# Optimization experiments

Hardware: AMD Instinct MI355X
Metric: run time of the kernel (lower is better)

Reference implementation:

```python
import jax, jax.numpy as jnp
import numpy as np

N = 100000      # nodes
E = 800000      # directed edges
D_IN = 128      # input features (n_inputs)
HIDDEN = 128    # conf['model']['hidden_size']
D_OUT = 2       # conv2 output classes


def setup_inputs() -> dict:
    key = jax.random.key(0)
    k0, k1, k2, k3 = jax.random.split(key, 4)
    x = jax.random.normal(k0, (N, D_IN), dtype=jnp.float32)
    edge_index = jax.random.randint(k1, (2, E), 0, N, dtype=jnp.int32)
    # Glorot-style init for GCNConv weights, zero bias (PyG defaults)
    s1 = float(np.sqrt(6.0 / (D_IN + HIDDEN)))
    s2 = float(np.sqrt(6.0 / (HIDDEN + D_OUT)))
    W1 = jax.random.uniform(k2, (D_IN, HIDDEN), jnp.float32, -s1, s1)
    b1 = jnp.zeros((HIDDEN,), jnp.float32)
    W2 = jax.random.uniform(k3, (HIDDEN, D_OUT), jnp.float32, -s2, s2)
    b2 = jnp.zeros((D_OUT,), jnp.float32)
    return {"x": x, "edge_index": edge_index, "W1": W1, "b1": b1, "W2": W2, "b2": b2}


def gcn_conv(x, src, dst, W, b):
    """PyG GCNConv: add self-loops, symmetric deg^-1/2 A deg^-1/2 normalization."""
    n = x.shape[0]
    h = x @ W                                                   # [N, F_out]
    ones_e = jnp.ones((src.shape[0],), h.dtype)
    # degree with self-loops (init to 1)
    deg = jnp.ones((n,), h.dtype).at[dst].add(ones_e)           # [N]
    dinv = 1.0 / jnp.sqrt(deg)
    norm = (dinv[src] * dinv[dst])[:, None]                     # [E, 1]
    # self-loop contribution: norm_ii = dinv_i^2; then scatter edge messages
    out = (h * (dinv * dinv)[:, None]).at[dst].add(h[src] * norm)
    return out + b


def reference(x, edge_index, W1, b1, W2, b2):
    src, dst = edge_index[0], edge_index[1]
    h = jax.nn.relu(gcn_conv(x, src, dst, W1, b1))
    return gcn_conv(h, src, dst, W2, b2)                        # [N, 2]
```

## Files before the change

kernel.cpp:

```cpp
#include <hip/hip_runtime.h>
#include <hip/hip_bf16.h>


#define D1 128
#define BSH 9
#define BSZ (1 << BSH)
#define CHA 2048

typedef __attribute__((ext_vector_type(8))) short short8;
typedef __attribute__((ext_vector_type(4))) float floatx4;

__device__ __forceinline__ unsigned short f2bf(float f) {
    unsigned u = __float_as_uint(f);
    u += 0x7fff + ((u >> 16) & 1);
    return (unsigned short)(u >> 16);
}
__device__ __forceinline__ float bflo(unsigned u) { return __uint_as_float(u << 16); }
__device__ __forceinline__ float bfhi(unsigned u) { return __uint_as_float(u & 0xffff0000u); }
__device__ __forceinline__ int clampN(int s, int N) {
    return (int)min((unsigned)s, (unsigned)N);
}

__global__ void k_init(const float* __restrict__ W1, unsigned short* __restrict__ W1t,
                       int* __restrict__ bcur, unsigned short* __restrict__ h1s,
                       float* __restrict__ h2s, int N) {
    int i = blockIdx.x * 256 + threadIdx.x;
    if (i < 256) bcur[i] = 0;
    if (i < D1) h1s[(size_t)N * D1 + i] = 0;
    if (i < 2)  h2s[(size_t)N * 2 + i] = 0.f;
    if (i < D1 * D1) {
        int c = i >> 7, k = i & 127;
        W1t[c * D1 + k] = f2bf(W1[k * D1 + c]);
    }
}

__global__ __launch_bounds__(256) void k_binA(
    const int* __restrict__ src, const int* __restrict__ dst,
    int* __restrict__ bcur, unsigned* __restrict__ packed, int E, int nbuck, int CAP)
{
    __shared__ int hist[256];
    __shared__ int cur[256];
    const int t = threadIdx.x;
    const int e0 = blockIdx.x * CHA;
    const int e1 = min(e0 + CHA, E);

    for (int i = t; i < nbuck; i += 256) hist[i] = 0;
    __syncthreads();
    for (int i = e0 + t; i < e1; i += 256)
        atomicAdd(&hist[dst[i] >> BSH], 1);
    __syncthreads();
    for (int i = t; i < nbuck; i += 256)
        cur[i] = (hist[i] > 0) ? atomicAdd(&bcur[i], hist[i]) : 0;
    __syncthreads();
    for (int i = e0 + t; i < e1; i += 256) {
        int d = dst[i];
        int b = d >> BSH;
        int pos = atomicAdd(&cur[b], 1);
        if (pos < CAP)
            packed[(size_t)b * CAP + pos] = ((unsigned)src[i] << BSH) | (unsigned)(d & (BSZ - 1));
    }
}

__global__ __launch_bounds__(512) void k_binB(
    const int* __restrict__ bcur, const unsigned* __restrict__ packed,
    int2* __restrict__ rp, float* __restrict__ dinv,
    int* __restrict__ esrc, int* __restrict__ order, int N, int CAP)
{
    __shared__ int lh[BSZ];
    __shared__ int lcur[BSZ];
    __shared__ int wsum[8];
    __shared__ int dbin[64];
    __shared__ int dcur[64];

    const int t = threadIdx.x;
    const int s = blockIdx.x << BSH;
    const int n = min(BSZ, N - s);
    const int base = blockIdx.x * CAP;
    const int cnt = min(bcur[blockIdx.x], CAP);

    lh[t] = 0;
    if (t < 64) dbin[t] = 0;
    __syncthreads();
    for (int i = t; i < cnt; i += 512)
        atomicAdd(&lh[packed[base + i] & (BSZ - 1)], 1);
    __syncthreads();

    const int deg = lh[t];
    const int pdeg = (deg + 3) & ~3;

    int inc = pdeg;
#pragma unroll
    for (int off = 1; off < 64; off <<= 1) {
        int u = __shfl_up(inc, off);
        if ((t & 63) >= off) inc += u;
    }
    if ((t & 63) == 63) wsum[t >> 6] = inc;
    __syncthreads();
    if (t < 8) {
        int w = wsum[t];
#pragma unroll
        for (int off = 1; off < 8; off <<= 1) {
            int u = __shfl_up(w, off, 8);
            if ((t & 7) >= off) w += u;
        }
        wsum[t] = w;
    }
    __syncthreads();
    int excl = ((t >> 6) ? wsum[(t >> 6) - 1] : 0) + inc - pdeg;

    if (t < n) {
        rp[s + t] = make_int2(base + excl, deg);
        dinv[s + t] = rsqrtf(1.0f + (float)deg);
        atomicAdd(&dbin[63 - min(deg, 63)], 1);
        for (int k = deg; k < pdeg; ++k) {
            int p = excl + k;
            if (p < CAP) esrc[base + p] = N;
        }
    }
    lcur[t] = excl;
    __syncthreads();

    for (int i = t; i < cnt; i += 512) {
        unsigned p = packed[base + i];
        int ld = (int)(p & (BSZ - 1));
        int pos = atomicAdd(&lcur[ld], 1);
        if (pos < CAP) esrc[base + pos] = (int)(p >> BSH);
    }

    __syncthreads();
    if (t < 64) {
        int dv = dbin[t];
        int dinc = dv;
#pragma unroll
        for (int off = 1; off < 64; off <<= 1) {
            int u = __shfl_up(dinc, off);
            if (t >= off) dinc += u;
        }
        dcur[t] = dinc - dv;
    }
    __syncthreads();
    if (t < n) {
        int b = 63 - min(deg, 63);
        int pos = atomicAdd(&dcur[b], 1);
        order[s + pos] = s + t;
    }
}

#define BMM 64
__global__ __launch_bounds__(256) void k_gemm1(
    const float* __restrict__ x, const unsigned short* __restrict__ W1t,
    const float* __restrict__ dinv, unsigned short* __restrict__ h1s, int N)
{
    __shared__ unsigned short Xs[BMM][136];
    __shared__ unsigned short Ws[D1][136];

    const int t = threadIdx.x;
    const int row0 = blockIdx.x * BMM;

#pragma unroll
    for (int i = 0; i < 8; ++i) {
        int idx = t + 256 * i;
        int r = idx >> 4, c8 = idx & 15;
        short8 v = ((const short8*)W1t)[r * 16 + c8];
        *(short8*)&Ws[r][c8 * 8] = v;
    }
#pragma unroll
    for (int i = 0; i < 4; ++i) {
        int idx = t + 256 * i;
        int r = idx >> 4, c8 = idx & 15;
        int row = row0 + r;
        short8 v8 = (short8)0;
        if (row < N) {
            const float* p = x + (size_t)row * D1 + c8 * 8;
            float4 f0 = *(const float4*)p;
            float4 f1 = *(const float4*)(p + 4);
            v8[0] = (short)f2bf(f0.x); v8[1] = (short)f2bf(f0.y);
            v8[2] = (short)f2bf(f0.z); v8[3] = (short)f2bf(f0.w);
            v8[4] = (short)f2bf(f1.x); v8[5] = (short)f2bf(f1.y);
            v8[6] = (short)f2bf(f1.z); v8[7] = (short)f2bf(f1.w);
        }
        *(short8*)&Xs[r][c8 * 8] = v8;
    }
    __syncthreads();

    const int w = t >> 6;
    const int l = t & 63;
    const int m = l & 15;
    const int q = l >> 4;

    floatx4 acc[8];
#pragma unroll
    for (int c = 0; c < 8; ++c) acc[c] = (floatx4)0.0f;

#pragma unroll
    for (int ks = 0; ks < 4; ++ks) {
        short8 a = *(const short8*)&Xs[16 * w + m][ks * 32 + q * 8];
#pragma unroll
        for (int c = 0; c < 8; ++c) {
            short8 b = *(const short8*)&Ws[c * 16 + m][ks * 32 + q * 8];
            acc[c] = __builtin_amdgcn_mfma_f32_16x16x32_bf16(a, b, acc[c], 0, 0, 0);
        }
    }

    __syncthreads();

#pragma unroll
    for (int r = 0; r < 4; ++r) {
        int rt = 16 * w + q * 4 + r;
        int row = row0 + rt;
        float di = (row < N) ? dinv[row] : 0.f;
#pragma unroll
        for (int c = 0; c < 8; ++c)
            Xs[rt][c * 16 + m] = f2bf(acc[c][r] * di);
    }
    __syncthreads();

#pragma unroll
    for (int i = 0; i < 4; ++i) {
        int idx = t + 256 * i;
        int r = idx >> 4, c8 = idx & 15;
        int row = row0 + r;
        if (row < N)
            *(short8*)&h1s[(size_t)row * D1 + c8 * 8] = *(const short8*)&Xs[r][c8 * 8];
    }
}

#define ACC8(A, v) \
    A[0] += bflo(v.x); A[1] += bfhi(v.x); \
    A[2] += bflo(v.y); A[3] += bfhi(v.y); \
    A[4] += bflo(v.z); A[5] += bfhi(v.z); \
    A[6] += bflo(v.w); A[7] += bfhi(v.w);

__global__ __launch_bounds__(256) void k_agg1_gemm2(
    const int2* __restrict__ rp, const int* __restrict__ esrc,
    const int* __restrict__ order,
    const float* __restrict__ dinv, const unsigned short* __restrict__ h1s,
    const float* __restrict__ b1, const float* __restrict__ W2,
    float* __restrict__ h2s, int N)
{
    int gid = blockIdx.x * 256 + threadIdx.x;
    int grp = gid >> 4;
    if (grp >= N) return;
    int node = order[grp];
    int lane = gid & 15;

    const uint4* h1v = (const uint4*)h1s;
    const int4*  ev  = (const int4*)esrc;

    uint4 u = h1v[(size_t)node * 16 + lane];
    float accA[8], accB[8];
    accA[0] = bflo(u.x); accA[1] = bfhi(u.x);
    accA[2] = bflo(u.y); accA[3] = bfhi(u.y);
    accA[4] = bflo(u.z); accA[5] = bfhi(u.z);
    accA[6] = bflo(u.w); accA[7] = bfhi(u.w);
#pragma unroll
    for (int j = 0; j < 8; ++j) accB[j] = 0.f;

    int2 r = rp[node];
    int beg = r.x;
    int end4 = beg + ((r.y + 3) & ~3);

    for (int e = beg; e < end4; e += 8) {
        int q = e >> 2;
        int4 i0 = ev[q];
        int4 i1 = ev[q + 1];
        bool c1 = (e + 4) < end4;
        int s0 = clampN(i0.x, N), s1 = clampN(i0.y, N);
        int s2 = clampN(i0.z, N), s3 = clampN(i0.w, N);
        int s4 = c1 ? clampN(i1.x, N) : N, s5 = c1 ? clampN(i1.y, N) : N;
        int s6 = c1 ? clampN(i1.z, N) : N, s7 = c1 ? clampN(i1.w, N) : N;
        uint4 v0 = h1v[(size_t)s0 * 16 + lane];
        uint4 v1 = h1v[(size_t)s1 * 16 + lane];
        uint4 v2 = h1v[(size_t)s2 * 16 + lane];
        uint4 v3 = h1v[(size_t)s3 * 16 + lane];
        uint4 v4 = h1v[(size_t)s4 * 16 + lane];
        uint4 v5 = h1v[(size_t)s5 * 16 + lane];
        uint4 v6 = h1v[(size_t)s6 * 16 + lane];
        uint4 v7 = h1v[(size_t)s7 * 16 + lane];
        ACC8(accA, v0) ACC8(accB, v1) ACC8(accA, v2) ACC8(accB, v3)
        ACC8(accA, v4) ACC8(accB, v5) ACC8(accA, v6) ACC8(accB, v7)
    }

    float di = dinv[node];
    const float4* b1v = (const float4*)b1;
    float4 bbA = b1v[lane * 2 + 0];
    float4 bbB = b1v[lane * 2 + 1];
    float a[8];
    a[0] = fmaxf((accA[0] + accB[0]) * di + bbA.x, 0.f);
    a[1] = fmaxf((accA[1] + accB[1]) * di + bbA.y, 0.f);
    a[2] = fmaxf((accA[2] + accB[2]) * di + bbA.z, 0.f);
    a[3] = fmaxf((accA[3] + accB[3]) * di + bbA.w, 0.f);
    a[4] = fmaxf((accA[4] + accB[4]) * di + bbB.x, 0.f);
    a[5] = fmaxf((accA[5] + accB[5]) * di + bbB.y, 0.f);
    a[6] = fmaxf((accA[6] + accB[6]) * di + bbB.z, 0.f);
    a[7] = fmaxf((accA[7] + accB[7]) * di + bbB.w, 0.f);

    const float4* W2v = (const float4*)W2;
    float p0 = 0.f, p1 = 0.f;
#pragma unroll
    for (int j2 = 0; j2 < 4; ++j2) {
        float4 wv = W2v[lane * 4 + j2];
        p0 += a[j2 * 2] * wv.x + a[j2 * 2 + 1] * wv.z;
        p1 += a[j2 * 2] * wv.y + a[j2 * 2 + 1] * wv.w;
    }

#pragma unroll
    for (int off = 8; off > 0; off >>= 1) {
        p0 += __shfl_xor(p0, off);
        p1 += __shfl_xor(p1, off);
    }
    if (lane == 0) {
        h2s[(size_t)node * 2 + 0] = p0 * di;
        h2s[(size_t)node * 2 + 1] = p1 * di;
    }
}

__global__ void k_gather2(const int2* __restrict__ rp, const int* __restrict__ esrc,
                          const float* __restrict__ h2s, const float* __restrict__ dinv,
                          const float* __restrict__ b2, float* __restrict__ out, int N)
{
    int i = blockIdx.x * 256 + threadIdx.x;
    if (i >= N) return;
    const float2* h2v = (const float2*)h2s;
    const int4* ev = (const int4*)esrc;
    float2 h = h2v[i];
    float o0a = h.x, o1a = h.y;
    float o0b = 0.f, o1b = 0.f;
    int2 r = rp[i];
    int beg = r.x;
    int end4 = beg + ((r.y + 3) & ~3);
    for (int e = beg; e < end4; e += 8) {
        int q = e >> 2;
        int4 i0 = ev[q];
        int4 i1 = ev[q + 1];
        bool c1 = (e + 4) < end4;
        int s0 = clampN(i0.x, N), s1 = clampN(i0.y, N);
        int s2 = clampN(i0.z, N), s3 = clampN(i0.w, N);
        int s4 = c1 ? clampN(i1.x, N) : N, s5 = c1 ? clampN(i1.y, N) : N;
        int s6 = c1 ? clampN(i1.z, N) : N, s7 = c1 ? clampN(i1.w, N) : N;
        float2 v0 = h2v[s0], v1 = h2v[s1], v2 = h2v[s2], v3 = h2v[s3];
        float2 v4 = h2v[s4], v5 = h2v[s5], v6 = h2v[s6], v7 = h2v[s7];
        o0a += v0.x + v2.x + v4.x + v6.x; o1a += v0.y + v2.y + v4.y + v6.y;
        o0b += v1.x + v3.x + v5.x + v7.x; o1b += v1.y + v3.y + v5.y + v7.y;
    }
    float di = dinv[i];
    ((float2*)out)[i] = make_float2((o0a + o0b) * di + b2[0], (o1a + o1b) * di + b2[1]);
}

extern "C" void kernel_launch(void* const* d_in, const int* in_sizes, int n_in,
                              void* d_out, int out_size, void* d_ws, size_t ws_size,
                              hipStream_t stream)
{
    const float* x  = (const float*)d_in[0];
    const int*   ei = (const int*)d_in[1];
    const float* W1 = (const float*)d_in[2];
    const float* b1 = (const float*)d_in[3];
    const float* W2 = (const float*)d_in[4];
    const float* b2 = (const float*)d_in[5];
    float* out = (float*)d_out;

    const int N = in_sizes[0] / D1;
    const int E = in_sizes[1] / 2;
    const int* src = ei;
    const int* dst = ei + E;

    const int nbuck = (N + BSZ - 1) >> BSH;
    const int avg = (E + nbuck - 1) / nbuck;
    const int CAP = (2 * avg + 3 * BSZ + 63) & ~63;

    char* w = (char*)d_ws;
    auto alloc = [&](size_t bytes) -> char* {
        char* r = w;
        w += (bytes + 63) & ~(size_t)63;
        return r;
    };
    unsigned short* h1s = (unsigned short*)alloc((size_t)(N + 1) * D1 * 2);
    unsigned short* W1t = (unsigned short*)alloc((size_t)D1 * D1 * 2);
    float* h2s    = (float*)alloc((size_t)(N + 1) * 2 * 4);
    float* dinv   = (float*)alloc((size_t)N * 4);
    int2*  rp     = (int2*)alloc((size_t)N * 8);
    int*   order  = (int*)alloc((size_t)N * 4);
    int*   bcur   = (int*)alloc(256 * 4);
    unsigned* packed = (unsigned*)alloc((size_t)nbuck * CAP * 4);
    int*   esrc   = (int*)alloc(((size_t)nbuck * CAP + 256) * 4);

    k_init <<<(D1 * D1 + 255) / 256, 256, 0, stream>>>(W1, W1t, bcur, h1s, h2s, N);
    k_binA <<<(E + CHA - 1) / CHA, 256, 0, stream>>>(src, dst, bcur, packed, E, nbuck, CAP);
    k_binB <<<nbuck, 512, 0, stream>>>(bcur, packed, rp, dinv, esrc, order, N, CAP);

    k_gemm1<<<(N + BMM - 1) / BMM, 256, 0, stream>>>(x, W1t, dinv, h1s, N);

    k_agg1_gemm2<<<(N * 16 + 255) / 256, 256, 0, stream>>>(rp, esrc, order, dinv, h1s, b1, W2, h2s, N);

    k_gather2<<<(N + 255) / 256, 256, 0, stream>>>(rp, esrc, h2s, dinv, b2, out, N);
}
```

Baseline: 181.0 us.

## Shrink bucket size, enlarge GEMM tile, and widen gather2 unrolling

Halves the destination bucket size so binning uses about 391 buckets of 256 nodes (with bucket arrays sized up to 1024), giving k_binB more, smaller blocks. k_gemm1 moves to 128-row tiles with 512 threads. k_gather2 processes 16 edges per iteration to raise memory-level parallelism. These are three separate tuning changes. Register pressure and the Xs tile sizing in gemm1 for the larger tile are possible risks.

Result: no change. 180.8 us (-0.1%).

```diff
diff --git a/kernel.cpp b/kernel.cpp
--- a/kernel.cpp
+++ b/kernel.cpp
@@ -3,8 +3,9 @@
 
 
 #define D1 128
-#define BSH 9
+#define BSH 8
 #define BSZ (1 << BSH)
+#define NBMAX 1024
 #define CHA 2048
 
 typedef __attribute__((ext_vector_type(8))) short short8;
@@ -25,7 +26,7 @@
                        int* __restrict__ bcur, unsigned short* __restrict__ h1s,
                        float* __restrict__ h2s, int N) {
     int i = blockIdx.x * 256 + threadIdx.x;
-    if (i < 256) bcur[i] = 0;
+    if (i < NBMAX) bcur[i] = 0;
     if (i < D1) h1s[(size_t)N * D1 + i] = 0;
     if (i < 2)  h2s[(size_t)N * 2 + i] = 0.f;
     if (i < D1 * D1) {
@@ -38,8 +39,8 @@
     const int* __restrict__ src, const int* __restrict__ dst,
     int* __restrict__ bcur, unsigned* __restrict__ packed, int E, int nbuck, int CAP)
 {
-    __shared__ int hist[256];
-    __shared__ int cur[256];
+    __shared__ int hist[NBMAX];
+    __shared__ int cur[NBMAX];
     const int t = threadIdx.x;
     const int e0 = blockIdx.x * CHA;
     const int e1 = min(e0 + CHA, E);
@@ -61,14 +62,14 @@
     }
 }
 
-__global__ __launch_bounds__(512) void k_binB(
+__global__ __launch_bounds__(BSZ) void k_binB(
     const int* __restrict__ bcur, const unsigned* __restrict__ packed,
     int2* __restrict__ rp, float* __restrict__ dinv,
     int* __restrict__ esrc, int* __restrict__ order, int N, int CAP)
 {
     __shared__ int lh[BSZ];
     __shared__ int lcur[BSZ];
-    __shared__ int wsum[8];
+    __shared__ int wsum[BSZ / 64];
     __shared__ int dbin[64];
     __shared__ int dcur[64];
 
@@ -81,7 +82,7 @@
     lh[t] = 0;
     if (t < 64) dbin[t] = 0;
     __syncthreads();
-    for (int i = t; i < cnt; i += 512)
+    for (int i = t; i < cnt; i += BSZ)
         atomicAdd(&lh[packed[base + i] & (BSZ - 1)], 1);
     __syncthreads();
 
@@ -96,12 +97,12 @@
     }
     if ((t & 63) == 63) wsum[t >> 6] = inc;
     __syncthreads();
-    if (t < 8) {
+    if (t < BSZ / 64) {
         int w = wsum[t];
 #pragma unroll
-        for (int off = 1; off < 8; off <<= 1) {
-            int u = __shfl_up(w, off, 8);
-            if ((t & 7) >= off) w += u;
+        for (int off = 1; off < BSZ / 64; off <<= 1) {
+            int u = __shfl_up(w, off, BSZ / 64);
+            if ((t & (BSZ / 64 - 1)) >= off) w += u;
         }
         wsum[t] = w;
     }
@@ -120,7 +121,7 @@
     lcur[t] = excl;
     __syncthreads();
 
-    for (int i = t; i < cnt; i += 512) {
+    for (int i = t; i < cnt; i += BSZ) {
         unsigned p = packed[base + i];
         int ld = (int)(p & (BSZ - 1));
         int pos = atomicAdd(&lcur[ld], 1);
@@ -146,8 +147,8 @@
     }
 }
 
-#define BMM 64
-__global__ __launch_bounds__(256) void k_gemm1(
+#define BMM 128
+__global__ __launch_bounds__(512) void k_gemm1(
     const float* __restrict__ x, const unsigned short* __restrict__ W1t,
     const float* __restrict__ dinv, unsigned short* __restrict__ h1s, int N)
 {
@@ -158,15 +159,15 @@
     const int row0 = blockIdx.x * BMM;
 
 #pragma unroll
-    for (int i = 0; i < 8; ++i) {
-        int idx = t + 256 * i;
+    for (int i = 0; i < 4; ++i) {
+        int idx = t + 512 * i;
         int r = idx >> 4, c8 = idx & 15;
         short8 v = ((const short8*)W1t)[r * 16 + c8];
         *(short8*)&Ws[r][c8 * 8] = v;
     }
 #pragma unroll
     for (int i = 0; i < 4; ++i) {
-        int idx = t + 256 * i;
+        int idx = t + 512 * i;
         int r = idx >> 4, c8 = idx & 15;
         int row = row0 + r;
         short8 v8 = (short8)0;
@@ -217,7 +218,7 @@
 
 #pragma unroll
     for (int i = 0; i < 4; ++i) {
-        int idx = t + 256 * i;
+        int idx = t + 512 * i;
         int r = idx >> 4, c8 = idx & 15;
         int row = row0 + r;
         if (row < N)
@@ -329,19 +330,29 @@
     int2 r = rp[i];
     int beg = r.x;
     int end4 = beg + ((r.y + 3) & ~3);
-    for (int e = beg; e < end4; e += 8) {
+    for (int e = beg; e < end4; e += 16) {
         int q = e >> 2;
         int4 i0 = ev[q];
         int4 i1 = ev[q + 1];
-        bool c1 = (e + 4) < end4;
+        int4 i2 = ev[q + 2];
+        int4 i3 = ev[q + 3];
+        bool c1 = (e + 4) < end4, c2 = (e + 8) < end4, c3 = (e + 12) < end4;
         int s0 = clampN(i0.x, N), s1 = clampN(i0.y, N);
         int s2 = clampN(i0.z, N), s3 = clampN(i0.w, N);
         int s4 = c1 ? clampN(i1.x, N) : N, s5 = c1 ? clampN(i1.y, N) : N;
         int s6 = c1 ? clampN(i1.z, N) : N, s7 = c1 ? clampN(i1.w, N) : N;
+        int s8 = c2 ? clampN(i2.x, N) : N, s9 = c2 ? clampN(i2.y, N) : N;
+        int sa = c2 ? clampN(i2.z, N) : N, sb = c2 ? clampN(i2.w, N) : N;
+        int sc = c3 ? clampN(i3.x, N) : N, sd = c3 ? clampN(i3.y, N) : N;
+        int se = c3 ? clampN(i3.z, N) : N, sf = c3 ? clampN(i3.w, N) : N;
         float2 v0 = h2v[s0], v1 = h2v[s1], v2 = h2v[s2], v3 = h2v[s3];
         float2 v4 = h2v[s4], v5 = h2v[s5], v6 = h2v[s6], v7 = h2v[s7];
-        o0a += v0.x + v2.x + v4.x + v6.x; o1a += v0.y + v2.y + v4.y + v6.y;
-        o0b += v1.x + v3.x + v5.x + v7.x; o1b += v1.y + v3.y + v5.y + v7.y;
+        float2 v8 = h2v[s8], v9 = h2v[s9], va = h2v[sa], vb = h2v[sb];
+        float2 vc = h2v[sc], vd = h2v[sd], ve = h2v[se], vf = h2v[sf];
+        o0a += v0.x + v2.x + v4.x + v6.x + v8.x + va.x + vc.x + ve.x;
+        o1a += v0.y + v2.y + v4.y + v6.y + v8.y + va.y + vc.y + ve.y;
+        o0b += v1.x + v3.x + v5.x + v7.x + v9.x + vb.x + vd.x + vf.x;
+        o1b += v1.y + v3.y + v5.y + v7.y + v9.y + vb.y + vd.y + vf.y;
     }
     float di = dinv[i];
     ((float2*)out)[i] = make_float2((o0a + o0b) * di + b2[0], (o1a + o1b) * di + b2[1]);
@@ -380,15 +391,15 @@
     float* dinv   = (float*)alloc((size_t)N * 4);
     int2*  rp     = (int2*)alloc((size_t)N * 8);
     int*   order  = (int*)alloc((size_t)N * 4);
-    int*   bcur   = (int*)alloc(256 * 4);
+    int*   bcur   = (int*)alloc(NBMAX * 4);
     unsigned* packed = (unsigned*)alloc((size_t)nbuck * CAP * 4);
     int*   esrc   = (int*)alloc(((size_t)nbuck * CAP + 256) * 4);
 
     k_init <<<(D1 * D1 + 255) / 256, 256, 0, stream>>>(W1, W1t, bcur, h1s, h2s, N);
     k_binA <<<(E + CHA - 1) / CHA, 256, 0, stream>>>(src, dst, bcur, packed, E, nbuck, CAP);
-    k_binB <<<nbuck, 512, 0, stream>>>(bcur, packed, rp, dinv, esrc, order, N, CAP);
-
-    k_gemm1<<<(N + BMM - 1) / BMM, 256, 0, stream>>>(x, W1t, dinv, h1s, N);
+    k_binB <<<nbuck, BSZ, 0, stream>>>(bcur, packed, rp, dinv, esrc, order, N, CAP);
+
+    k_gemm1<<<(N + BMM - 1) / BMM, 512, 0, stream>>>(x, W1t, dinv, h1s, N);
 
     k_agg1_gemm2<<<(N * 16 + 255) / 256, 256, 0, stream>>>(rp, esrc, order, dinv, h1s, b1, W2, h2s, N);
 
```
